# Optimization experiments

Hardware: AMD Instinct MI355X
Metric: run time of the kernel (lower is better)

Reference implementation:

```python
import jax, jax.numpy as jnp
import numpy as np
from functools import partial

MAX_DEPTH = 100.0
MIN_DEPTH = 0.1
KS = 5  # custom_kernel_size


def _dilate(x, k):
    # max_pool2d(x, k, stride=1, padding=k//2); torch pads with -inf for max pool
    p = k // 2
    return jax.lax.reduce_window(x, -jnp.inf, jax.lax.max,
                                 (1, 1, k, k), (1, 1, 1, 1),
                                 [(0, 0), (0, 0), (p, p), (p, p)])


def _erode(x, k):
    return -_dilate(-x, k)


def _median_blur(x, k):
    # torch impl: conv2d with identity kernels (zero padding) then median over window dim
    p = k // 2
    b, c, h, w = x.shape
    xp = jnp.pad(x, ((0, 0), (0, 0), (p, p), (p, p)))  # zeros, matching conv2d padding
    wins = jnp.stack([xp[:, :, i:i + h, j:j + w]
                      for i in range(k) for j in range(k)], axis=2)  # [b,c,k*k,h,w]
    return jnp.median(wins, axis=2)


def _gaussian_blur5(x):
    # torchvision gaussian_blur(kernel_size=5, sigma=None):
    # sigma = 0.3*((5-1)*0.5 - 1) + 0.8 = 1.1, reflect padding
    sigma = 1.1
    r = jnp.arange(5, dtype=x.dtype) - 2.0
    g1 = jnp.exp(-(r ** 2) / (2.0 * sigma ** 2))
    g1 = g1 / jnp.sum(g1)
    g2 = jnp.outer(g1, g1)  # [5,5]
    xp = jnp.pad(x, ((0, 0), (0, 0), (2, 2), (2, 2)), mode='reflect')
    kern = g2[None, None]  # [O=1, I=1, 5, 5]
    return jax.lax.conv_general_dilated(xp, kern, (1, 1), 'VALID',
                                        dimension_numbers=('NCHW', 'OIHW', 'NCHW'))


def setup_inputs() -> dict:
    key = jax.random.key(0)
    k1, k2 = jax.random.split(key)
    depth = jax.random.uniform(k1, (16, 1, 352, 1216), dtype=jnp.float32) * MAX_DEPTH
    mask = jax.random.uniform(k2, (16, 1, 352, 1216)) < 0.3
    in_depth = jnp.where(mask, depth, 0.0).astype(jnp.float32)
    return {"in_depth": in_depth}


def reference(in_depth):
    # invert
    dm = jnp.where(in_depth > MIN_DEPTH, MAX_DEPTH - in_depth, in_depth)
    # dilation with custom kernel
    dm = _dilate(dm, KS)
    # closing(5) = erode(dilate)
    dm = _erode(_dilate(dm, 5), 5)
    # fill empty pixels with 7x7 dilation
    empty = dm < MIN_DEPTH
    dm = jnp.where(empty, _dilate(dm, 7), dm)
    # median blur 5
    dm = _median_blur(dm, 5)
    # gaussian blur 5 on valid pixels
    blurred = _gaussian_blur5(dm)
    dm = jnp.where(dm > MIN_DEPTH, blurred, dm)
    # invert back
    dm = jnp.where(dm > MIN_DEPTH, MAX_DEPTH - dm, dm)
    return dm
```

## Files before the change

### kernel.cpp

```cpp
#include <hip/hip_runtime.h>
#include <float.h>

#define IW 1216
#define IH 352
#define W4 304
#define NF4 (16 * IH * W4)
#define MIND 0.1f
#define MAXD 100.0f

__device__ __forceinline__ float4 vmax4(float4 a, float4 b) {
    return make_float4(fmaxf(a.x,b.x), fmaxf(a.y,b.y), fmaxf(a.z,b.z), fmaxf(a.w,b.w));
}
__device__ __forceinline__ float4 vmin4(float4 a, float4 b) {
    return make_float4(fminf(a.x,b.x), fminf(a.y,b.y), fminf(a.z,b.z), fminf(a.w,b.w));
}

__global__ __launch_bounds__(256) void morph_k(const float4* __restrict__ in,
                                               float4* __restrict__ out) {
    __shared__ float A_[50][152];
    __shared__ float B_[50][152];
    int b  = blockIdx.x;
    int sw = (b & 7) * 220 + (b >> 3);
    int tx = sw % 10; int t2 = sw / 10;
    int ty = t2 % 11; int n  = t2 / 11;
    int x0 = tx * 128, y0 = ty * 32;
    int tid = threadIdx.x;
    const int base4 = (x0 >> 2) - 3;
    const long ib = (long)n * IH * W4;

    for (int i = tid; i < 50 * 38; i += 256) {
        int r = i / 38, c4 = i % 38;
        int gy = y0 - 9 + r; int gx4 = base4 + c4;
        float4 v;
        if ((unsigned)gy < IH && (unsigned)gx4 < (unsigned)W4) {
            v = in[ib + gy * W4 + gx4];
            v.x = v.x > MIND ? MAXD - v.x : v.x;
            v.y = v.y > MIND ? MAXD - v.y : v.y;
            v.z = v.z > MIND ? MAXD - v.z : v.z;
            v.w = v.w > MIND ? MAXD - v.w : v.w;
        } else { v.x = v.y = v.z = v.w = -FLT_MAX; }
        *(float4*)&A_[r][c4 * 4] = v;
    }
    __syncthreads();

    for (int i = tid; i < 50 * 36; i += 256) {
        int r = i / 36, c = ((i % 36) + 1) * 4;
        float t[12];
        *(float4*)&t[0] = *(float4*)&A_[r][c - 4];
        *(float4*)&t[4] = *(float4*)&A_[r][c];
        *(float4*)&t[8] = *(float4*)&A_[r][c + 4];
        float cm  = fmaxf(fmaxf(fmaxf(t[3],t[4]), fmaxf(t[5],t[6])), fmaxf(t[7],t[8]));
        float m12 = fmaxf(t[1], t[2]);
        float m910= fmaxf(t[9], t[10]);
        float4 o;
        o.x = fmaxf(fmaxf(cm, t[0]),  m12);
        o.y = fmaxf(fmaxf(cm, t[9]),  m12);
        o.z = fmaxf(fmaxf(cm, t[2]),  m910);
        o.w = fmaxf(fmaxf(cm, t[11]), m910);
        *(float4*)&B_[r][c] = o;
    }
    __syncthreads();

    for (int i = tid; i < 42 * 36; i += 256) {
        int r = i / 36 + 4, c = ((i % 36) + 1) * 4;
        float4 m = *(float4*)&B_[r - 4][c];
        #pragma unroll
        for (int d = -3; d <= 4; ++d) m = vmax4(m, *(float4*)&B_[r + d][c]);
        *(float4*)&A_[r][c] = m;
    }
    __syncthreads();

    for (int i = tid; i < 42 * 36; i += 256) {
        int r = i / 36 + 4, c = ((i % 36) + 1) * 4;
        int gy = y0 - 9 + r; int gxb = x0 - 12 + c;
        bool rok = (unsigned)gy < IH;
        float4 v = *(float4*)&A_[r][c];
        v.x = (rok && (unsigned)(gxb + 0) < IW) ? v.x : FLT_MAX;
        v.y = (rok && (unsigned)(gxb + 1) < IW) ? v.y : FLT_MAX;
        v.z = (rok && (unsigned)(gxb + 2) < IW) ? v.z : FLT_MAX;
        v.w = (rok && (unsigned)(gxb + 3) < IW) ? v.w : FLT_MAX;
        *(float4*)&A_[r][c] = v;
    }
    __syncthreads();

    for (int i = tid; i < 42 * 34; i += 256) {
        int r = i / 34 + 4, c = ((i % 34) + 2) * 4;
        float t[12];
        *(float4*)&t[0] = *(float4*)&A_[r][c - 4];
        *(float4*)&t[4] = *(float4*)&A_[r][c];
        *(float4*)&t[8] = *(float4*)&A_[r][c + 4];
        float m34 = fminf(t[3], t[4]), m56 = fminf(t[5], t[6]), m78 = fminf(t[7], t[8]);
        float s  = fminf(m34, m56), s2 = fminf(m56, m78);
        float4 o;
        o.x = fminf(s,  t[2]);
        o.y = fminf(s,  t[7]);
        o.z = fminf(t[4], s2);
        o.w = fminf(s2, t[9]);
        *(float4*)&B_[r][c] = o;
    }
    __syncthreads();

    for (int i = tid; i < 38 * 34; i += 256) {
        int r = i / 34 + 6, c = ((i % 34) + 2) * 4;
        float4 m = *(float4*)&B_[r - 2][c];
        #pragma unroll
        for (int d = -1; d <= 2; ++d) m = vmin4(m, *(float4*)&B_[r + d][c]);
        *(float4*)&A_[r][c] = m;
    }
    __syncthreads();

    for (int i = tid; i < 38 * 34; i += 256) {
        int r = i / 34 + 6, c = ((i % 34) + 2) * 4;
        int gy = y0 - 9 + r; int gxb = x0 - 12 + c;
        bool rok = (unsigned)gy < IH;
        float4 v = *(float4*)&A_[r][c];
        v.x = (rok && (unsigned)(gxb + 0) < IW) ? v.x : -FLT_MAX;
        v.y = (rok && (unsigned)(gxb + 1) < IW) ? v.y : -FLT_MAX;
        v.z = (rok && (unsigned)(gxb + 2) < IW) ? v.z : -FLT_MAX;
        v.w = (rok && (unsigned)(gxb + 3) < IW) ? v.w : -FLT_MAX;
        *(float4*)&A_[r][c] = v;
    }
    __syncthreads();

    for (int i = tid; i < 38 * 32; i += 256) {
        int r = i / 32 + 6, c = ((i % 32) + 3) * 4;
        float t[12];
        *(float4*)&t[0] = *(float4*)&A_[r][c - 4];
        *(float4*)&t[4] = *(float4*)&A_[r][c];
        *(float4*)&t[8] = *(float4*)&A_[r][c + 4];
        float m23 = fmaxf(t[2], t[3]), m45 = fmaxf(t[4], t[5]);
        float m67 = fmaxf(t[6], t[7]), m89 = fmaxf(t[8], t[9]);
        float s = fmaxf(m45, m67);
        float sm23 = fmaxf(s, m23), sm89 = fmaxf(s, m89);
        float4 o;
        o.x = fmaxf(sm23, t[1]);
        o.y = fmaxf(sm23, t[8]);
        o.z = fmaxf(sm89, t[3]);
        o.w = fmaxf(sm89, t[10]);
        *(float4*)&B_[r][c] = o;
    }
    __syncthreads();

    for (int i = tid; i < 32 * 32; i += 256) {
        int r = i / 32 + 9, c = ((i % 32) + 3) * 4;
        float4 m = *(float4*)&B_[r - 3][c];
        #pragma unroll
        for (int d = -2; d <= 3; ++d) m = vmax4(m, *(float4*)&B_[r + d][c]);
        float4 cl = *(float4*)&A_[r][c];
        float4 o;
        o.x = cl.x < MIND ? m.x : cl.x;
        o.y = cl.y < MIND ? m.y : cl.y;
        o.z = cl.z < MIND ? m.z : cl.z;
        o.w = cl.w < MIND ? m.w : cl.w;
        int gy = y0 + r - 9;
        int gx4 = (x0 >> 2) + ((c - 12) >> 2);
        if (gx4 < W4) out[ib + gy * W4 + gx4] = o;
    }
}

#define CE(a,b) { float _l = fminf(a,b), _h = fmaxf(a,b); a = _l; b = _h; }
#define SORT5(a,b,c,d,e) { CE(a,b) CE(d,e) CE(c,e) CE(c,d) CE(a,d) CE(a,c) CE(b,e) CE(b,d) CE(b,c) }
#define MM8(s0,s1,s2,s3,s4,s5,s6,s7) { CE(s0,s1) CE(s2,s3) CE(s4,s5) CE(s6,s7) \
    CE(s0,s2) CE(s0,s4) CE(s0,s6) CE(s1,s7) CE(s3,s7) CE(s5,s7) }
#define MM7(s0,s1,s2,s3,s4,s5,s6) { CE(s0,s1) CE(s2,s3) CE(s4,s5) \
    CE(s0,s2) CE(s0,s4) CE(s0,s6) CE(s1,s6) CE(s3,s6) CE(s5,s6) }

__global__ __launch_bounds__(256) void median_k(const float4* __restrict__ in,
                                                float4* __restrict__ out) {
    int b  = blockIdx.x;
    int sb = (b & 7) * 836 + (b >> 3);
    int id = sb * 256 + threadIdx.x;
    int x4 = id % W4;
    int y  = (id / W4) % IH;

    float c8[8][5];
    const float4 z4 = make_float4(0.f, 0.f, 0.f, 0.f);
    #pragma unroll
    for (int r = 0; r < 5; ++r) {
        int yy = y + r - 2;
        bool ok = (unsigned)yy < IH;
        int rid = id + (r - 2) * W4;
        float4 L = (ok && x4 > 0)      ? in[rid - 1] : z4;
        float4 M = ok                  ? in[rid]     : z4;
        float4 R = (ok && x4 < W4 - 1) ? in[rid + 1] : z4;
        c8[0][r] = L.z; c8[1][r] = L.w;
        c8[2][r] = M.x; c8[3][r] = M.y; c8[4][r] = M.z; c8[5][r] = M.w;
        c8[6][r] = R.x; c8[7][r] = R.y;
    }
    #pragma unroll
    for (int j = 0; j < 8; ++j) SORT5(c8[j][0], c8[j][1], c8[j][2], c8[j][3], c8[j][4]);

    float res[4];
    #pragma unroll
    for (int p = 0; p < 4; ++p) {
        float m[5][5];
        #pragma unroll
        for (int i2 = 0; i2 < 5; ++i2) {
            #pragma unroll
            for (int j = 0; j < 5; ++j) m[i2][j] = c8[p + j][i2];
            SORT5(m[i2][0], m[i2][1], m[i2][2], m[i2][3], m[i2][4]);
        }
        float s0 = m[0][3], s1 = m[0][4], s2 = m[1][2], s3 = m[1][3];
        float s4 = m[1][4], s5 = m[2][1], s6 = m[2][2], s7 = m[2][3];
        MM8(s0,s1,s2,s3,s4,s5,s6,s7)
        s0 = m[3][0]; s7 = m[3][1];
        MM8(s0,s1,s2,s3,s4,s5,s6,s7)
        s0 = m[3][2]; s7 = m[4][0];
        MM8(s0,s1,s2,s3,s4,s5,s6,s7)
        s0 = m[4][1];
        MM7(s0,s1,s2,s3,s4,s5,s6)
        CE(s1,s2) CE(s3,s4) CE(s1,s3) CE(s2,s4)
        float mn = fminf(s2, s3), mx = fmaxf(s2, s3);
        res[p] = fmaxf(mn, fminf(mx, s5));
    }
    out[id] = make_float4(res[0], res[1], res[2], res[3]);
}

__global__ __launch_bounds__(256) void gauss_k(const float* __restrict__ dm,
                                               float4* __restrict__ out,
                                               float w0, float w1, float w2) {
    __shared__ float A3[36][136];
    __shared__ float B3[36][136];
    int b  = blockIdx.x;
    int sw = (b & 7) * 220 + (b >> 3);
    int tx = sw % 10; int t2 = sw / 10;
    int ty = t2 % 11; int n  = t2 / 11;
    int x0 = tx * 128, y0 = ty * 32;
    int tid = threadIdx.x;
    const long ibF = (long)n * IH * IW;

    for (int i = tid; i < 36 * 34; i += 256) {
        int r = i / 34, c4 = i % 34;
        int gy = y0 - 2 + r;
        gy = gy < 0 ? -gy : (gy >= IH ? 2 * IH - 2 - gy : gy);
        int gxb = x0 - 4 + c4 * 4;
        float4 v;
        if (gxb >= 0 && gxb + 3 < IW) {
            v = *(const float4*)&dm[ibF + (long)gy * IW + gxb];
        } else {
            float* pv = &v.x;
            #pragma unroll
            for (int k = 0; k < 4; ++k) {
                int gx = gxb + k;
                gx = gx < 0 ? -gx : (gx >= IW ? 2 * IW - 2 - gx : gx);
                pv[k] = dm[ibF + (long)gy * IW + gx];
            }
        }
        *(float4*)&A3[r][c4 * 4] = v;
    }
    __syncthreads();

    for (int i = tid; i < 36 * 32; i += 256) {
        int r = i / 32, c = ((i % 32) + 1) * 4;
        float t[12];
        *(float4*)&t[0] = *(float4*)&A3[r][c - 4];
        *(float4*)&t[4] = *(float4*)&A3[r][c];
        *(float4*)&t[8] = *(float4*)&A3[r][c + 4];
        float4 o;
        o.x = w2 * (t[2] + t[6]) + w1 * (t[3] + t[5]) + w0 * t[4];
        o.y = w2 * (t[3] + t[7]) + w1 * (t[4] + t[6]) + w0 * t[5];
        o.z = w2 * (t[4] + t[8]) + w1 * (t[5] + t[7]) + w0 * t[6];
        o.w = w2 * (t[5] + t[9]) + w1 * (t[6] + t[8]) + w0 * t[7];
        *(float4*)&B3[r][c] = o;
    }
    __syncthreads();

    for (int i = tid; i < 32 * 32; i += 256) {
        int r = i / 32 + 2, c = ((i % 32) + 1) * 4;
        float4 a = *(float4*)&B3[r - 2][c];
        float4 bb = *(float4*)&B3[r - 1][c];
        float4 cm = *(float4*)&B3[r][c];
        float4 d  = *(float4*)&B3[r + 1][c];
        float4 e  = *(float4*)&B3[r + 2][c];
        float4 bl;
        bl.x = w2 * (a.x + e.x) + w1 * (bb.x + d.x) + w0 * cm.x;
        bl.y = w2 * (a.y + e.y) + w1 * (bb.y + d.y) + w0 * cm.y;
        bl.z = w2 * (a.z + e.z) + w1 * (bb.z + d.z) + w0 * cm.z;
        bl.w = w2 * (a.w + e.w) + w1 * (bb.w + d.w) + w0 * cm.w;
        float4 med = *(float4*)&A3[r][c];
        float4 o;
        { float s = med.x > MIND ? bl.x : med.x; o.x = s > MIND ? MAXD - s : s; }
        { float s = med.y > MIND ? bl.y : med.y; o.y = s > MIND ? MAXD - s : s; }
        { float s = med.z > MIND ? bl.z : med.z; o.z = s > MIND ? MAXD - s : s; }
        { float s = med.w > MIND ? bl.w : med.w; o.w = s > MIND ? MAXD - s : s; }
        int gy = y0 + r - 2;
        int gx4 = (x0 >> 2) + ((c - 4) >> 2);
        if (gx4 < W4) out[(long)n * IH * W4 + gy * W4 + gx4] = o;
    }
}

extern "C" void kernel_launch(void* const* d_in, const int* in_sizes, int n_in,
                              void* d_out, int out_size, void* d_ws, size_t ws_size,
                              hipStream_t stream) {
    const float4* in = (const float4*)d_in[0];
    float4* W1 = (float4*)d_ws;
    float4* W2 = W1 + NF4;
    float4* O  = (float4*)d_out;

    float c2 = 2.42f;
    float e1 = expf(-1.0f / c2);
    float e4 = expf(-4.0f / c2);
    float s  = 1.0f + 2.0f * e1 + 2.0f * e4;
    float w0 = 1.0f / s, w1 = e1 / s, w2 = e4 / s;

    morph_k <<<dim3(1760), dim3(256), 0, stream>>>(in, W1);
    median_k<<<dim3(6688), dim3(256), 0, stream>>>(W1, W2);
    gauss_k <<<dim3(1760), dim3(256), 0, stream>>>((const float*)W2, O, w0, w1, w2);
}
```

Before: 193.5 us.

## Fuse morphology, median and gaussian stages into one tiled kernel

Merges the three kernels (morphology, median blur, gaussian blur) into a single kernel working on 24-row tiles with a 13-row halo, keeping every intermediate in shared memory. This removes the two global-memory round trips through workspace and two kernel launches. Vertical passes now use per-thread sliding windows down columns, and boundary masking is folded into the horizontal passes. The cost is large halo recomputation (50 rows loaded for 24 output rows) and heavier register use in the in-kernel median, which may reduce occupancy.

```diff
diff --git a/kernel.cpp b/kernel.cpp
--- a/kernel.cpp
+++ b/kernel.cpp
@@ -1,12 +1,13 @@
 #include <hip/hip_runtime.h>
 #include <float.h>
+#include <math.h>
 
 #define IW 1216
 #define IH 352
 #define W4 304
-#define NF4 (16 * IH * W4)
 #define MIND 0.1f
 #define MAXD 100.0f
+#define RB 50
 
 __device__ __forceinline__ float4 vmax4(float4 a, float4 b) {
     return make_float4(fmaxf(a.x,b.x), fmaxf(a.y,b.y), fmaxf(a.z,b.z), fmaxf(a.w,b.w));
@@ -15,277 +16,287 @@
     return make_float4(fminf(a.x,b.x), fminf(a.y,b.y), fminf(a.z,b.z), fminf(a.w,b.w));
 }
 
-__global__ __launch_bounds__(256) void morph_k(const float4* __restrict__ in,
-                                               float4* __restrict__ out) {
-    __shared__ float A_[50][152];
-    __shared__ float B_[50][152];
+#define CE(a,b) { float _l = fminf(a,b), _h = fmaxf(a,b); a = _l; b = _h; }
+#define SORT5(a,b,c,d,e) { CE(a,b) CE(d,e) CE(c,e) CE(c,d) CE(a,d) CE(a,c) CE(b,e) CE(b,d) CE(b,c) }
+#define MM8(s0,s1,s2,s3,s4,s5,s6,s7) { CE(s0,s1) CE(s2,s3) CE(s4,s5) CE(s6,s7) \
+    CE(s0,s2) CE(s0,s4) CE(s0,s6) CE(s1,s7) CE(s3,s7) CE(s5,s7) }
+#define MM7(s0,s1,s2,s3,s4,s5,s6) { CE(s0,s1) CE(s2,s3) CE(s4,s5) \
+    CE(s0,s2) CE(s0,s4) CE(s0,s6) CE(s1,s6) CE(s3,s6) CE(s5,s6) }
+
+__global__ __launch_bounds__(256, 2) void mega_k(const float4* __restrict__ in,
+                                                 float4* __restrict__ out,
+                                                 float w0, float w1, float w2) {
+    __shared__ float4 A_[RB][40];
+    __shared__ float4 B_[RB][38];
     int b  = blockIdx.x;
-    int sw = (b & 7) * 220 + (b >> 3);
+    int sw = (b & 7) * 300 + (b >> 3);
     int tx = sw % 10; int t2 = sw / 10;
-    int ty = t2 % 11; int n  = t2 / 11;
-    int x0 = tx * 128, y0 = ty * 32;
+    int ty = t2 % 15; int n  = t2 / 15;
+    int x0 = tx * 128, y0 = ty * 24;
     int tid = threadIdx.x;
-    const int base4 = (x0 >> 2) - 3;
-    const long ib = (long)n * IH * W4;
-
-    for (int i = tid; i < 50 * 38; i += 256) {
-        int r = i / 38, c4 = i % 38;
-        int gy = y0 - 9 + r; int gx4 = base4 + c4;
+    const long ib = (long)n * (IH * W4);
+    const int xb4 = x0 >> 2;
+
+    for (int i = tid; i < 50 * 40; i += 256) {
+        int ra = i / 40, ca = i % 40;
+        int gy = y0 + ra - 13, gx4 = xb4 + ca - 4;
         float4 v;
-        if ((unsigned)gy < IH && (unsigned)gx4 < (unsigned)W4) {
+        if ((unsigned)gy < IH && (unsigned)gx4 < W4) {
             v = in[ib + gy * W4 + gx4];
             v.x = v.x > MIND ? MAXD - v.x : v.x;
             v.y = v.y > MIND ? MAXD - v.y : v.y;
             v.z = v.z > MIND ? MAXD - v.z : v.z;
             v.w = v.w > MIND ? MAXD - v.w : v.w;
         } else { v.x = v.y = v.z = v.w = -FLT_MAX; }
-        *(float4*)&A_[r][c4 * 4] = v;
-    }
-    __syncthreads();
-
-    for (int i = tid; i < 50 * 36; i += 256) {
-        int r = i / 36, c = ((i % 36) + 1) * 4;
+        A_[ra][ca] = v;
+    }
+    __syncthreads();
+
+    for (int i = tid; i < 50 * 38; i += 256) {
+        int ra = i / 38, cb = i % 38;
         float t[12];
-        *(float4*)&t[0] = *(float4*)&A_[r][c - 4];
-        *(float4*)&t[4] = *(float4*)&A_[r][c];
-        *(float4*)&t[8] = *(float4*)&A_[r][c + 4];
-        float cm  = fmaxf(fmaxf(fmaxf(t[3],t[4]), fmaxf(t[5],t[6])), fmaxf(t[7],t[8]));
-        float m12 = fmaxf(t[1], t[2]);
-        float m910= fmaxf(t[9], t[10]);
+        *(float4*)&t[0] = A_[ra][cb];
+        *(float4*)&t[4] = A_[ra][cb + 1];
+        *(float4*)&t[8] = A_[ra][cb + 2];
+        float core = fmaxf(fmaxf(fmaxf(t[3],t[4]), fmaxf(t[5],t[6])), fmaxf(t[7],t[8]));
+        float a12 = fmaxf(t[1], t[2]), a910 = fmaxf(t[9], t[10]);
         float4 o;
-        o.x = fmaxf(fmaxf(cm, t[0]),  m12);
-        o.y = fmaxf(fmaxf(cm, t[9]),  m12);
-        o.z = fmaxf(fmaxf(cm, t[2]),  m910);
-        o.w = fmaxf(fmaxf(cm, t[11]), m910);
-        *(float4*)&B_[r][c] = o;
+        o.x = fmaxf(fmaxf(core, a12), t[0]);
+        o.y = fmaxf(fmaxf(core, a12), t[9]);
+        o.z = fmaxf(fmaxf(core, t[2]), a910);
+        o.w = fmaxf(fmaxf(core, a910), t[11]);
+        B_[ra][cb] = o;
+    }
+    __syncthreads();
+
+    {
+        int c = tid % 38, k = tid / 38;
+        if (k < 6) {
+            int ra0 = 4 + 7 * k;
+            float4 w[9];
+            #pragma unroll
+            for (int j = 0; j < 8; ++j) w[j] = B_[ra0 - 4 + j][c];
+            #pragma unroll
+            for (int s = 0; s < 7; ++s) {
+                w[8] = B_[ra0 + 4 + s][c];
+                float4 m = w[0];
+                #pragma unroll
+                for (int j = 1; j < 9; ++j) m = vmax4(m, w[j]);
+                A_[ra0 + s][c + 1] = m;
+                #pragma unroll
+                for (int j = 0; j < 8; ++j) w[j] = w[j + 1];
+            }
+        }
     }
     __syncthreads();
 
     for (int i = tid; i < 42 * 36; i += 256) {
-        int r = i / 36 + 4, c = ((i % 36) + 1) * 4;
-        float4 m = *(float4*)&B_[r - 4][c];
+        int ra = i / 36 + 4, cb = i % 36;
+        float t[12];
+        *(float4*)&t[0] = A_[ra][cb + 1];
+        *(float4*)&t[4] = A_[ra][cb + 2];
+        *(float4*)&t[8] = A_[ra][cb + 3];
+        bool rOK = (unsigned)(y0 + ra - 13) < IH;
         #pragma unroll
-        for (int d = -3; d <= 4; ++d) m = vmax4(m, *(float4*)&B_[r + d][c]);
-        *(float4*)&A_[r][c] = m;
-    }
-    __syncthreads();
-
-    for (int i = tid; i < 42 * 36; i += 256) {
-        int r = i / 36 + 4, c = ((i % 36) + 1) * 4;
-        int gy = y0 - 9 + r; int gxb = x0 - 12 + c;
-        bool rok = (unsigned)gy < IH;
-        float4 v = *(float4*)&A_[r][c];
-        v.x = (rok && (unsigned)(gxb + 0) < IW) ? v.x : FLT_MAX;
-        v.y = (rok && (unsigned)(gxb + 1) < IW) ? v.y : FLT_MAX;
-        v.z = (rok && (unsigned)(gxb + 2) < IW) ? v.z : FLT_MAX;
-        v.w = (rok && (unsigned)(gxb + 3) < IW) ? v.w : FLT_MAX;
-        *(float4*)&A_[r][c] = v;
-    }
-    __syncthreads();
-
-    for (int i = tid; i < 42 * 34; i += 256) {
-        int r = i / 34 + 4, c = ((i % 34) + 2) * 4;
+        for (int kk = 2; kk <= 9; ++kk) {
+            int gx = x0 + 4 * cb - 12 + kk;
+            t[kk] = (rOK && (unsigned)gx < IW) ? t[kk] : FLT_MAX;
+        }
+        float m34 = fminf(t[3], t[4]), m56 = fminf(t[5], t[6]), m78 = fminf(t[7], t[8]);
+        float4 o;
+        o.x = fminf(fminf(t[2], m34), m56);
+        o.y = fminf(fminf(m34, m56), t[7]);
+        o.z = fminf(fminf(t[4], m56), m78);
+        o.w = fminf(fminf(m56, m78), t[9]);
+        B_[ra][cb + 1] = o;
+    }
+    __syncthreads();
+
+    {
+        int c = tid % 36, k = tid / 36;
+        if (k < 7) {
+            int ra0 = 6 + 6 * k;
+            int rlen = min(6, 44 - ra0);
+            float4 w[5];
+            #pragma unroll
+            for (int j = 0; j < 4; ++j) w[j] = B_[ra0 - 2 + j][c + 1];
+            #pragma unroll
+            for (int s = 0; s < 6; ++s) {
+                if (s < rlen) {
+                    w[4] = B_[ra0 + 2 + s][c + 1];
+                    float4 m = w[0];
+                    #pragma unroll
+                    for (int j = 1; j < 5; ++j) m = vmin4(m, w[j]);
+                    A_[ra0 + s][c + 2] = m;
+                    #pragma unroll
+                    for (int j = 0; j < 4; ++j) w[j] = w[j + 1];
+                }
+            }
+        }
+    }
+    __syncthreads();
+
+    for (int i = tid; i < 38 * 34; i += 256) {
+        int ra = i / 34 + 6, cb2 = i % 34;
         float t[12];
-        *(float4*)&t[0] = *(float4*)&A_[r][c - 4];
-        *(float4*)&t[4] = *(float4*)&A_[r][c];
-        *(float4*)&t[8] = *(float4*)&A_[r][c + 4];
-        float m34 = fminf(t[3], t[4]), m56 = fminf(t[5], t[6]), m78 = fminf(t[7], t[8]);
-        float s  = fminf(m34, m56), s2 = fminf(m56, m78);
+        *(float4*)&t[0] = A_[ra][cb2 + 2];
+        *(float4*)&t[4] = A_[ra][cb2 + 3];
+        *(float4*)&t[8] = A_[ra][cb2 + 4];
+        bool rOK = (unsigned)(y0 + ra - 13) < IH;
+        #pragma unroll
+        for (int kk = 1; kk <= 10; ++kk) {
+            int gx = x0 + 4 * cb2 - 8 + kk;
+            t[kk] = (rOK && (unsigned)gx < IW) ? t[kk] : -FLT_MAX;
+        }
+        float core = fmaxf(fmaxf(t[4], t[5]), fmaxf(t[6], t[7]));
+        float a23 = fmaxf(t[2], t[3]), a89 = fmaxf(t[8], t[9]);
         float4 o;
-        o.x = fminf(s,  t[2]);
-        o.y = fminf(s,  t[7]);
-        o.z = fminf(t[4], s2);
-        o.w = fminf(s2, t[9]);
-        *(float4*)&B_[r][c] = o;
-    }
-    __syncthreads();
-
-    for (int i = tid; i < 38 * 34; i += 256) {
-        int r = i / 34 + 6, c = ((i % 34) + 2) * 4;
-        float4 m = *(float4*)&B_[r - 2][c];
-        #pragma unroll
-        for (int d = -1; d <= 2; ++d) m = vmin4(m, *(float4*)&B_[r + d][c]);
-        *(float4*)&A_[r][c] = m;
-    }
-    __syncthreads();
-
-    for (int i = tid; i < 38 * 34; i += 256) {
-        int r = i / 34 + 6, c = ((i % 34) + 2) * 4;
-        int gy = y0 - 9 + r; int gxb = x0 - 12 + c;
-        bool rok = (unsigned)gy < IH;
-        float4 v = *(float4*)&A_[r][c];
-        v.x = (rok && (unsigned)(gxb + 0) < IW) ? v.x : -FLT_MAX;
-        v.y = (rok && (unsigned)(gxb + 1) < IW) ? v.y : -FLT_MAX;
-        v.z = (rok && (unsigned)(gxb + 2) < IW) ? v.z : -FLT_MAX;
-        v.w = (rok && (unsigned)(gxb + 3) < IW) ? v.w : -FLT_MAX;
-        *(float4*)&A_[r][c] = v;
-    }
-    __syncthreads();
-
-    for (int i = tid; i < 38 * 32; i += 256) {
-        int r = i / 32 + 6, c = ((i % 32) + 3) * 4;
+        o.x = fmaxf(fmaxf(core, a23), t[1]);
+        o.y = fmaxf(fmaxf(core, a23), t[8]);
+        o.z = fmaxf(fmaxf(core, t[3]), a89);
+        o.w = fmaxf(fmaxf(core, a89), t[10]);
+        B_[ra][cb2 + 2] = o;
+    }
+    __syncthreads();
+
+    {
+        int c = tid % 34, k = tid / 34;
+        if (k < 7) {
+            int ra0 = 9 + 5 * k;
+            int rlen = min(5, 41 - ra0);
+            float4 w[7];
+            #pragma unroll
+            for (int j = 0; j < 6; ++j) w[j] = B_[ra0 - 3 + j][c + 2];
+            #pragma unroll
+            for (int s = 0; s < 5; ++s) {
+                if (s < rlen) {
+                    w[6] = B_[ra0 + 3 + s][c + 2];
+                    float4 m = w[0];
+                    #pragma unroll
+                    for (int j = 1; j < 7; ++j) m = vmax4(m, w[j]);
+                    float4 cl = A_[ra0 + s][c + 3];
+                    float4 o;
+                    o.x = cl.x < MIND ? m.x : cl.x;
+                    o.y = cl.y < MIND ? m.y : cl.y;
+                    o.z = cl.z < MIND ? m.z : cl.z;
+                    o.w = cl.w < MIND ? m.w : cl.w;
+                    A_[ra0 + s][c + 3] = o;
+                    #pragma unroll
+                    for (int j = 0; j < 6; ++j) w[j] = w[j + 1];
+                }
+            }
+        }
+    }
+    __syncthreads();
+
+    {
+        int c = tid % 34, k = tid / 34;
+        if (k < 7) {
+            int ra0 = 11 + 4 * k;
+            float rows_[5][8];
+            auto loadrow = [&](float* rw, int rr) {
+                float4 q0 = A_[rr][c + 2], q1 = A_[rr][c + 3], q2 = A_[rr][c + 4];
+                float tmp[8] = {q0.z, q0.w, q1.x, q1.y, q1.z, q1.w, q2.x, q2.y};
+                bool rOK = (unsigned)(y0 + rr - 13) < IH;
+                #pragma unroll
+                for (int j = 0; j < 8; ++j) {
+                    int gx = x0 + 4 * c - 6 + j;
+                    rw[j] = (rOK && (unsigned)gx < IW) ? tmp[j] : 0.0f;
+                }
+            };
+            #pragma unroll
+            for (int j = 0; j < 4; ++j) loadrow(rows_[j], ra0 - 2 + j);
+            #pragma unroll
+            for (int st = 0; st < 4; ++st) {
+                loadrow(rows_[4], ra0 + 2 + st);
+                float cs[8][5];
+                #pragma unroll
+                for (int j = 0; j < 8; ++j) {
+                    float a0 = rows_[0][j], a1 = rows_[1][j], a2 = rows_[2][j],
+                          a3 = rows_[3][j], a4 = rows_[4][j];
+                    SORT5(a0, a1, a2, a3, a4)
+                    cs[j][0] = a0; cs[j][1] = a1; cs[j][2] = a2; cs[j][3] = a3; cs[j][4] = a4;
+                }
+                float rr4[4];
+                #pragma unroll
+                for (int p = 0; p < 4; ++p) {
+                    float m[5][5];
+                    #pragma unroll
+                    for (int i2 = 0; i2 < 5; ++i2) {
+                        m[i2][0] = cs[p][i2];     m[i2][1] = cs[p + 1][i2];
+                        m[i2][2] = cs[p + 2][i2]; m[i2][3] = cs[p + 3][i2];
+                        m[i2][4] = cs[p + 4][i2];
+                        SORT5(m[i2][0], m[i2][1], m[i2][2], m[i2][3], m[i2][4])
+                    }
+                    float s0 = m[0][3], s1 = m[0][4], s2 = m[1][2], s3 = m[1][3];
+                    float s4 = m[1][4], s5 = m[2][1], s6 = m[2][2], s7 = m[2][3];
+                    MM8(s0, s1, s2, s3, s4, s5, s6, s7)
+                    s0 = m[3][0]; s7 = m[3][1];
+                    MM8(s0, s1, s2, s3, s4, s5, s6, s7)
+                    s0 = m[3][2]; s7 = m[4][0];
+                    MM8(s0, s1, s2, s3, s4, s5, s6, s7)
+                    s0 = m[4][1];
+                    MM7(s0, s1, s2, s3, s4, s5, s6)
+                    CE(s1, s2) CE(s3, s4) CE(s1, s3) CE(s2, s4)
+                    float mn = fminf(s2, s3), mx = fmaxf(s2, s3);
+                    rr4[p] = fmaxf(mn, fminf(mx, s5));
+                }
+                B_[ra0 + st][c + 2] = make_float4(rr4[0], rr4[1], rr4[2], rr4[3]);
+                #pragma unroll
+                for (int j = 0; j < 4; ++j) {
+                    #pragma unroll
+                    for (int q = 0; q < 8; ++q) rows_[j][q] = rows_[j + 1][q];
+                }
+            }
+        }
+    }
+    __syncthreads();
+
+    for (int i = tid; i < 28 * 32; i += 256) {
+        int ra = i / 32 + 11, cb3 = i % 32;
         float t[12];
-        *(float4*)&t[0] = *(float4*)&A_[r][c - 4];
-        *(float4*)&t[4] = *(float4*)&A_[r][c];
-        *(float4*)&t[8] = *(float4*)&A_[r][c + 4];
-        float m23 = fmaxf(t[2], t[3]), m45 = fmaxf(t[4], t[5]);
-        float m67 = fmaxf(t[6], t[7]), m89 = fmaxf(t[8], t[9]);
-        float s = fmaxf(m45, m67);
-        float sm23 = fmaxf(s, m23), sm89 = fmaxf(s, m89);
-        float4 o;
-        o.x = fmaxf(sm23, t[1]);
-        o.y = fmaxf(sm23, t[8]);
-        o.z = fmaxf(sm89, t[3]);
-        o.w = fmaxf(sm89, t[10]);
-        *(float4*)&B_[r][c] = o;
-    }
-    __syncthreads();
-
-    for (int i = tid; i < 32 * 32; i += 256) {
-        int r = i / 32 + 9, c = ((i % 32) + 3) * 4;
-        float4 m = *(float4*)&B_[r - 3][c];
-        #pragma unroll
-        for (int d = -2; d <= 3; ++d) m = vmax4(m, *(float4*)&B_[r + d][c]);
-        float4 cl = *(float4*)&A_[r][c];
-        float4 o;
-        o.x = cl.x < MIND ? m.x : cl.x;
-        o.y = cl.y < MIND ? m.y : cl.y;
-        o.z = cl.z < MIND ? m.z : cl.z;
-        o.w = cl.w < MIND ? m.w : cl.w;
-        int gy = y0 + r - 9;
-        int gx4 = (x0 >> 2) + ((c - 12) >> 2);
-        if (gx4 < W4) out[ib + gy * W4 + gx4] = o;
-    }
-}
-
-#define CE(a,b) { float _l = fminf(a,b), _h = fmaxf(a,b); a = _l; b = _h; }
-#define SORT5(a,b,c,d,e) { CE(a,b) CE(d,e) CE(c,e) CE(c,d) CE(a,d) CE(a,c) CE(b,e) CE(b,d) CE(b,c) }
-#define MM8(s0,s1,s2,s3,s4,s5,s6,s7) { CE(s0,s1) CE(s2,s3) CE(s4,s5) CE(s6,s7) \
-    CE(s0,s2) CE(s0,s4) CE(s0,s6) CE(s1,s7) CE(s3,s7) CE(s5,s7) }
-#define MM7(s0,s1,s2,s3,s4,s5,s6) { CE(s0,s1) CE(s2,s3) CE(s4,s5) \
-    CE(s0,s2) CE(s0,s4) CE(s0,s6) CE(s1,s6) CE(s3,s6) CE(s5,s6) }
-
-__global__ __launch_bounds__(256) void median_k(const float4* __restrict__ in,
-                                                float4* __restrict__ out) {
-    int b  = blockIdx.x;
-    int sb = (b & 7) * 836 + (b >> 3);
-    int id = sb * 256 + threadIdx.x;
-    int x4 = id % W4;
-    int y  = (id / W4) % IH;
-
-    float c8[8][5];
-    const float4 z4 = make_float4(0.f, 0.f, 0.f, 0.f);
-    #pragma unroll
-    for (int r = 0; r < 5; ++r) {
-        int yy = y + r - 2;
-        bool ok = (unsigned)yy < IH;
-        int rid = id + (r - 2) * W4;
-        float4 L = (ok && x4 > 0)      ? in[rid - 1] : z4;
-        float4 M = ok                  ? in[rid]     : z4;
-        float4 R = (ok && x4 < W4 - 1) ? in[rid + 1] : z4;
-        c8[0][r] = L.z; c8[1][r] = L.w;
-        c8[2][r] = M.x; c8[3][r] = M.y; c8[4][r] = M.z; c8[5][r] = M.w;
-        c8[6][r] = R.x; c8[7][r] = R.y;
-    }
-    #pragma unroll
-    for (int j = 0; j < 8; ++j) SORT5(c8[j][0], c8[j][1], c8[j][2], c8[j][3], c8[j][4]);
-
-    float res[4];
-    #pragma unroll
-    for (int p = 0; p < 4; ++p) {
-        float m[5][5];
-        #pragma unroll
-        for (int i2 = 0; i2 < 5; ++i2) {
-            #pragma unroll
-            for (int j = 0; j < 5; ++j) m[i2][j] = c8[p + j][i2];
-            SORT5(m[i2][0], m[i2][1], m[i2][2], m[i2][3], m[i2][4]);
-        }
-        float s0 = m[0][3], s1 = m[0][4], s2 = m[1][2], s3 = m[1][3];
-        float s4 = m[1][4], s5 = m[2][1], s6 = m[2][2], s7 = m[2][3];
-        MM8(s0,s1,s2,s3,s4,s5,s6,s7)
-        s0 = m[3][0]; s7 = m[3][1];
-        MM8(s0,s1,s2,s3,s4,s5,s6,s7)
-        s0 = m[3][2]; s7 = m[4][0];
-        MM8(s0,s1,s2,s3,s4,s5,s6,s7)
-        s0 = m[4][1];
-        MM7(s0,s1,s2,s3,s4,s5,s6)
-        CE(s1,s2) CE(s3,s4) CE(s1,s3) CE(s2,s4)
-        float mn = fminf(s2, s3), mx = fmaxf(s2, s3);
-        res[p] = fmaxf(mn, fminf(mx, s5));
-    }
-    out[id] = make_float4(res[0], res[1], res[2], res[3]);
-}
-
-__global__ __launch_bounds__(256) void gauss_k(const float* __restrict__ dm,
-                                               float4* __restrict__ out,
-                                               float w0, float w1, float w2) {
-    __shared__ float A3[36][136];
-    __shared__ float B3[36][136];
-    int b  = blockIdx.x;
-    int sw = (b & 7) * 220 + (b >> 3);
-    int tx = sw % 10; int t2 = sw / 10;
-    int ty = t2 % 11; int n  = t2 / 11;
-    int x0 = tx * 128, y0 = ty * 32;
-    int tid = threadIdx.x;
-    const long ibF = (long)n * IH * IW;
-
-    for (int i = tid; i < 36 * 34; i += 256) {
-        int r = i / 34, c4 = i % 34;
-        int gy = y0 - 2 + r;
-        gy = gy < 0 ? -gy : (gy >= IH ? 2 * IH - 2 - gy : gy);
-        int gxb = x0 - 4 + c4 * 4;
-        float4 v;
-        if (gxb >= 0 && gxb + 3 < IW) {
-            v = *(const float4*)&dm[ibF + (long)gy * IW + gxb];
-        } else {
-            float* pv = &v.x;
-            #pragma unroll
-            for (int k = 0; k < 4; ++k) {
-                int gx = gxb + k;
-                gx = gx < 0 ? -gx : (gx >= IW ? 2 * IW - 2 - gx : gx);
-                pv[k] = dm[ibF + (long)gy * IW + gx];
-            }
-        }
-        *(float4*)&A3[r][c4 * 4] = v;
-    }
-    __syncthreads();
-
-    for (int i = tid; i < 36 * 32; i += 256) {
-        int r = i / 32, c = ((i % 32) + 1) * 4;
-        float t[12];
-        *(float4*)&t[0] = *(float4*)&A3[r][c - 4];
-        *(float4*)&t[4] = *(float4*)&A3[r][c];
-        *(float4*)&t[8] = *(float4*)&A3[r][c + 4];
+        *(float4*)&t[0] = B_[ra][cb3 + 2];
+        *(float4*)&t[4] = B_[ra][cb3 + 3];
+        *(float4*)&t[8] = B_[ra][cb3 + 4];
+        if (x0 == 0 && cb3 == 0)      { t[2] = t[6]; t[3] = t[5]; }
+        if (x0 == 1152 && cb3 == 15)  { t[8] = t[6]; t[9] = t[5]; }
         float4 o;
         o.x = w2 * (t[2] + t[6]) + w1 * (t[3] + t[5]) + w0 * t[4];
         o.y = w2 * (t[3] + t[7]) + w1 * (t[4] + t[6]) + w0 * t[5];
         o.z = w2 * (t[4] + t[8]) + w1 * (t[5] + t[7]) + w0 * t[6];
         o.w = w2 * (t[5] + t[9]) + w1 * (t[6] + t[8]) + w0 * t[7];
-        *(float4*)&B3[r][c] = o;
-    }
-    __syncthreads();
-
-    for (int i = tid; i < 32 * 32; i += 256) {
-        int r = i / 32 + 2, c = ((i % 32) + 1) * 4;
-        float4 a = *(float4*)&B3[r - 2][c];
-        float4 bb = *(float4*)&B3[r - 1][c];
-        float4 cm = *(float4*)&B3[r][c];
-        float4 d  = *(float4*)&B3[r + 1][c];
-        float4 e  = *(float4*)&B3[r + 2][c];
-        float4 bl;
-        bl.x = w2 * (a.x + e.x) + w1 * (bb.x + d.x) + w0 * cm.x;
-        bl.y = w2 * (a.y + e.y) + w1 * (bb.y + d.y) + w0 * cm.y;
-        bl.z = w2 * (a.z + e.z) + w1 * (bb.z + d.z) + w0 * cm.z;
-        bl.w = w2 * (a.w + e.w) + w1 * (bb.w + d.w) + w0 * cm.w;
-        float4 med = *(float4*)&A3[r][c];
-        float4 o;
-        { float s = med.x > MIND ? bl.x : med.x; o.x = s > MIND ? MAXD - s : s; }
-        { float s = med.y > MIND ? bl.y : med.y; o.y = s > MIND ? MAXD - s : s; }
-        { float s = med.z > MIND ? bl.z : med.z; o.z = s > MIND ? MAXD - s : s; }
-        { float s = med.w > MIND ? bl.w : med.w; o.w = s > MIND ? MAXD - s : s; }
-        int gy = y0 + r - 2;
-        int gx4 = (x0 >> 2) + ((c - 4) >> 2);
-        if (gx4 < W4) out[(long)n * IH * W4 + gy * W4 + gx4] = o;
+        A_[ra][cb3 + 4] = o;
+    }
+    __syncthreads();
+
+    {
+        int c = tid % 32, k = tid / 32;
+        int ra0 = 13 + 3 * k;
+        #pragma unroll
+        for (int s = 0; s < 3; ++s) {
+            int ra = ra0 + s;
+            int gy = y0 + ra - 13;
+            float4 acc = make_float4(0.f, 0.f, 0.f, 0.f);
+            #pragma unroll
+            for (int d = -2; d <= 2; ++d) {
+                int gy2 = gy + d;
+                gy2 = gy2 < 0 ? -gy2 : gy2;
+                gy2 = gy2 >= IH ? 2 * IH - 2 - gy2 : gy2;
+                int ra2 = gy2 - y0 + 13;
+                float4 hv = A_[ra2][c + 4];
+                float wd = (d == 0) ? w0 : ((d == 1 || d == -1) ? w1 : w2);
+                acc.x = fmaf(wd, hv.x, acc.x); acc.y = fmaf(wd, hv.y, acc.y);
+                acc.z = fmaf(wd, hv.z, acc.z); acc.w = fmaf(wd, hv.w, acc.w);
+            }
+            float4 dm = B_[ra][c + 3];
+            float4 o;
+            { float sv = dm.x > MIND ? acc.x : dm.x; o.x = sv > MIND ? MAXD - sv : sv; }
+            { float sv = dm.y > MIND ? acc.y : dm.y; o.y = sv > MIND ? MAXD - sv : sv; }
+            { float sv = dm.z > MIND ? acc.z : dm.z; o.z = sv > MIND ? MAXD - sv : sv; }
+            { float sv = dm.w > MIND ? acc.w : dm.w; o.w = sv > MIND ? MAXD - sv : sv; }
+            int gx4 = xb4 + c;
+            if (gy < IH && gx4 < W4) out[ib + (long)gy * W4 + gx4] = o;
+        }
     }
 }
 
@@ -293,9 +304,7 @@
                               void* d_out, int out_size, void* d_ws, size_t ws_size,
                               hipStream_t stream) {
     const float4* in = (const float4*)d_in[0];
-    float4* W1 = (float4*)d_ws;
-    float4* W2 = W1 + NF4;
-    float4* O  = (float4*)d_out;
+    float4* O = (float4*)d_out;
 
     float c2 = 2.42f;
     float e1 = expf(-1.0f / c2);
@@ -303,7 +312,5 @@
     float s  = 1.0f + 2.0f * e1 + 2.0f * e4;
     float w0 = 1.0f / s, w1 = e1 / s, w2 = e4 / s;
 
-    morph_k <<<dim3(1760), dim3(256), 0, stream>>>(in, W1);
-    median_k<<<dim3(6688), dim3(256), 0, stream>>>(W1, W2);
-    gauss_k <<<dim3(1760), dim3(256), 0, stream>>>((const float*)W2, O, w0, w1, w2);
+    mega_k<<<dim3(2400), dim3(256), 0, stream>>>(in, O, w0, w1, w2);
 }
```

Result: faster. 182.3 us (-5.8%).
